# Performance work log

Measured on AMD Instinct MI355X. Metric: run time of the kernel, lower is better.

## Reference

```python
import jax, jax.numpy as jnp
import numpy as np

B, S, D, H = 4, 2048, 1024, 16
DK = D // H


def setup_inputs() -> dict:
    key = jax.random.key(0)
    ks = jax.random.split(key, 11)
    inp = {
        'query': jax.random.normal(ks[0], (B, S, D), jnp.float32),
        'key': jax.random.normal(ks[1], (B, S, D), jnp.float32),
        'value': jax.random.normal(ks[2], (B, S, D), jnp.float32),
        'mask': jnp.tril(jnp.ones((1, 1, S, S), dtype=bool)),  # causal
    }
    sc = 1.0 / np.sqrt(D)
    inp['w_q'] = jax.random.normal(ks[3], (D, D), jnp.float32) * sc
    inp['b_q'] = jnp.zeros((D,), jnp.float32)
    inp['w_k'] = jax.random.normal(ks[4], (D, D), jnp.float32) * sc
    inp['b_k'] = jnp.zeros((D,), jnp.float32)
    inp['w_v'] = jax.random.normal(ks[5], (D, D), jnp.float32) * sc
    inp['b_v'] = jnp.zeros((D,), jnp.float32)
    inp['w_o'] = jax.random.normal(ks[6], (D, D), jnp.float32) * sc
    inp['b_o'] = jnp.zeros((D,), jnp.float32)
    return inp


def _split_heads(x):
    # Faithful to source: view(B, S, d_k, H) then permute(0,3,1,2)
    b, s, _ = x.shape
    return x.reshape(b, s, DK, H).transpose(0, 3, 1, 2)  # (B, H, S, DK)


def _concat_heads(x):
    # permute(0,2,1,3) -> reshape(B, S, d_k*H)
    b, h, s, dk = x.shape
    return x.transpose(0, 2, 1, 3).reshape(b, s, dk * h)


def reference(query, key, value, mask, w_q, b_q, w_k, b_k, w_v, b_v, w_o, b_o):
    q = query @ w_q.T + b_q
    k = key @ w_k.T + b_k
    v = value @ w_v.T + b_v
    q, k, v = _split_heads(q), _split_heads(k), _split_heads(v)
    scale = 1.0 / jnp.sqrt(jnp.asarray(DK, q.dtype))
    scores = jnp.einsum('bhqd,bhkd->bhqk', q, k) * scale
    scores = jnp.where(mask, scores, -jnp.inf)
    attn = jax.nn.softmax(scores, axis=-1)  # dropout p=0 -> identity
    out = jnp.einsum('bhqk,bhkd->bhqd', attn, v)
    return _concat_heads(out) @ w_o.T + b_o
```

## Files before the change

kernel.cpp:

```cpp
#include <hip/hip_runtime.h>

#define BB 4
#define SS 2048
#define DD 1024
#define HH 16
#define DK 64
#define MM (BB * SS)

typedef __bf16 bf16x8 __attribute__((ext_vector_type(8)));
typedef float f32x4 __attribute__((ext_vector_type(4)));
typedef unsigned short us8 __attribute__((ext_vector_type(8)));
typedef unsigned short us4 __attribute__((ext_vector_type(4)));

#define MFMA_BF16(a, b, c) __builtin_amdgcn_mfma_f32_16x16x32_bf16((a), (b), (c), 0, 0, 0)

__device__ __forceinline__ unsigned short f2bf(float f) {
  return __builtin_bit_cast(unsigned short, (__bf16)f);
}

__device__ __forceinline__ bf16x8 ld_frag(const unsigned short* p) {
  return __builtin_bit_cast(bf16x8, *(const us8*)p);
}

__device__ __forceinline__ void gl_lds16(const unsigned short* g, unsigned short* l) {
  __builtin_amdgcn_global_load_lds((const __attribute__((address_space(1))) void*)g,
                                   (__attribute__((address_space(3))) void*)l, 16, 0, 0);
}

__global__ void cvt_weights(const float* __restrict__ w0, const float* __restrict__ w1,
                            const float* __restrict__ w2, const float* __restrict__ w3,
                            unsigned short* __restrict__ dst) {
  const float* src = (blockIdx.y == 0) ? w0 : (blockIdx.y == 1) ? w1 : (blockIdx.y == 2) ? w2 : w3;
  unsigned short* d = dst + (size_t)blockIdx.y * (DD * DD);
  int idx = (blockIdx.x * 256 + threadIdx.x) * 4;
  float4 v = *(const float4*)(src + idx);
  us4 o;
  o[0] = f2bf(v.x); o[1] = f2bf(v.y); o[2] = f2bf(v.z); o[3] = f2bf(v.w);
  *(us4*)(d + idx) = o;
}

__global__ void cvt_act(const float* __restrict__ xq, const float* __restrict__ xk,
                        const float* __restrict__ xv, unsigned short* __restrict__ dq,
                        unsigned short* __restrict__ dk, unsigned short* __restrict__ dv) {
  const float* src = (blockIdx.y == 0) ? xq : (blockIdx.y == 1) ? xk : xv;
  unsigned short* dst = (blockIdx.y == 0) ? dq : (blockIdx.y == 1) ? dk : dv;
  int idx = (blockIdx.x * 256 + threadIdx.x) * 8;
  float4 a = *(const float4*)(src + idx);
  float4 b = *(const float4*)(src + idx + 4);
  us8 o;
  o[0] = f2bf(a.x); o[1] = f2bf(a.y); o[2] = f2bf(a.z); o[3] = f2bf(a.w);
  o[4] = f2bf(b.x); o[5] = f2bf(b.y); o[6] = f2bf(b.z); o[7] = f2bf(b.w);
  *(us8*)(dst + idx) = o;
}

__global__ __launch_bounds__(256, 4) void qkv_gemm_bf(
    const unsigned short* __restrict__ xb, const unsigned short* __restrict__ w,
    const float* __restrict__ bias, unsigned short* __restrict__ outp, int mode) {
  const int m0 = blockIdx.x * 128;
  const int h0 = blockIdx.y * 2;

  __shared__ unsigned short smem[17408];
  unsigned short* sA = smem;
  unsigned short* sB = smem + 8192;

  const int tid = threadIdx.x;
  const int lane = tid & 63;
  const int wave = tid >> 6;
  const int wm = wave & 1, wn = wave >> 1;
  const int quad = lane >> 4, l16 = lane & 15;

  f32x4 acc[4][4];
#pragma unroll
  for (int i = 0; i < 4; i++)
#pragma unroll
    for (int j = 0; j < 4; j++) acc[i][j] = f32x4{0.f, 0.f, 0.f, 0.f};

  for (int k0 = 0; k0 < DD; k0 += 64) {
    __syncthreads();
#pragma unroll
    for (int j = 0; j < 4; j++) {
      int cid = tid + j * 256;
      int half = cid >> 9, rr = (cid & 511) >> 2, c8 = (cid & 3) << 3;
      gl_lds16(xb + (size_t)(m0 + rr) * DD + k0 + half * 32 + c8,
               sA + half * 4096 + rr * 32 + c8);
    }
#pragma unroll
    for (int j = 0; j < 4; j++) {
      int cid = tid + j * 256;
      int half = cid >> 9, rr = (cid & 511) >> 2, c8 = (cid & 3) << 3;
      int n = ((rr & 63) << 4) + h0 + (rr >> 6);
      gl_lds16(w + (size_t)n * DD + k0 + half * 32 + c8,
               sB + half * 4096 + rr * 32 + c8);
    }
    __syncthreads();

#pragma unroll
    for (int kk = 0; kk < 2; kk++) {
      bf16x8 af[4];
#pragma unroll
      for (int mi = 0; mi < 4; mi++)
        af[mi] = ld_frag(sA + kk * 4096 + (wm * 64 + mi * 16 + l16) * 32 + quad * 8);
#pragma unroll
      for (int ni = 0; ni < 4; ni++) {
        bf16x8 bfr = ld_frag(sB + kk * 4096 + (wn * 64 + ni * 16 + l16) * 32 + quad * 8);
#pragma unroll
        for (int mi = 0; mi < 4; mi++) acc[mi][ni] = MFMA_BF16(af[mi], bfr, acc[mi][ni]);
      }
    }
  }

  if (mode < 2) {
#pragma unroll
    for (int mi = 0; mi < 4; mi++) {
#pragma unroll
      for (int ni = 0; ni < 4; ni++) {
        int c = wn * 64 + ni * 16 + l16;
        int h = h0 + (c >> 6), dk = c & 63;
        float bvv = bias[(dk << 4) + h];
        int mg0 = m0 + wm * 64 + mi * 16 + quad * 4;
#pragma unroll
        for (int r = 0; r < 4; r++) {
          int mg = mg0 + r;
          int bb = mg >> 11, s = mg & 2047;
          size_t dst = ((size_t)((bb << 4) + h) * SS + s) * DK + dk;
          outp[dst] = f2bf(acc[mi][ni][r] + bvv);
        }
      }
    }
  } else {
    __syncthreads();
#pragma unroll
    for (int mi = 0; mi < 4; mi++) {
#pragma unroll
      for (int ni = 0; ni < 4; ni++) {
        int c = wn * 64 + ni * 16 + l16;
        int h = h0 + (c >> 6), dk = c & 63;
        float bvv = bias[(dk << 4) + h];
        int ml0 = wm * 64 + mi * 16 + quad * 4;
#pragma unroll
        for (int r = 0; r < 4; r++)
          smem[c * 136 + ml0 + r] = f2bf(acc[mi][ni][r] + bvv);
      }
    }
    __syncthreads();
    int bb = m0 >> 11;
    int sbase = m0 & 2047;
#pragma unroll
    for (int i = 0; i < 8; i++) {
      int idx = tid + i * 256;
      int c = idx >> 4, mc = (idx & 15) << 3;
      int h = h0 + (c >> 6), dk = c & 63;
      size_t dst = ((size_t)((bb << 4) + h) * DK + dk) * SS + sbase + mc;
      *(us8*)(outp + dst) = *(const us8*)(smem + c * 136 + mc);
    }
  }
}

__global__ __launch_bounds__(256, 2) void attn(
    const unsigned short* __restrict__ qh, const unsigned short* __restrict__ kh,
    const unsigned short* __restrict__ vt, unsigned short* __restrict__ outc) {
  const int bh = blockIdx.x;
  const int by = blockIdx.y;
  const int b = bh >> 4, h = bh & 15;
  const unsigned short* Qp = qh + (size_t)bh * SS * DK;
  const unsigned short* Kp = kh + (size_t)bh * SS * DK;
  const unsigned short* Vp = vt + (size_t)bh * DK * SS;

  __shared__ unsigned short sK[128 * 72];
  __shared__ unsigned short sV[64 * 136];

  const int tid = threadIdx.x;
  const int lane = tid & 63;
  const int wave = tid >> 6;
  const int quad = lane >> 4, l16 = lane & 15;
  const int wq0 = wave * 32;

  const float sl = 0.125f * 1.44269504088896f;

  for (int pass = 0; pass < 2; pass++) {
    const int qt = pass ? (15 - by) : by;
    const int q0 = qt * 128;

    bf16x8 aq[2][2];
#pragma unroll
    for (int mi = 0; mi < 2; mi++)
#pragma unroll
      for (int kk = 0; kk < 2; kk++)
        aq[mi][kk] = ld_frag(Qp + (size_t)(q0 + wq0 + mi * 16 + l16) * DK + kk * 32 + quad * 8);

    f32x4 o_acc[2][4];
    float mrowL[2], lrowL[2];
#pragma unroll
    for (int mi = 0; mi < 2; mi++) {
#pragma unroll
      for (int ni = 0; ni < 4; ni++) o_acc[mi][ni] = f32x4{0.f, 0.f, 0.f, 0.f};
      mrowL[mi] = -1e30f;
      lrowL[mi] = 0.f;
    }

    for (int kt = 0; kt <= qt; kt++) {
      const int k0 = kt * 128;
      const bool diag = (kt == qt);
      __syncthreads();
#pragma unroll
      for (int i = 0; i < 4; i++) {
        int idx = tid + i * 256;
        int row = idx >> 3, c8 = (idx & 7) << 3;
        *(us8*)(sK + row * 72 + c8) = *(const us8*)(Kp + (size_t)(k0 + row) * DK + c8);
      }
#pragma unroll
      for (int i = 0; i < 4; i++) {
        int idx = tid + i * 256;
        int row = idx >> 4, cc = (idx & 15) << 3;
        *(us8*)(sV + row * 136 + cc) = *(const us8*)(Vp + (size_t)row * SS + k0 + cc);
      }
      __syncthreads();

      f32x4 sc[2][8];
#pragma unroll
      for (int mi = 0; mi < 2; mi++)
#pragma unroll
        for (int kti = 0; kti < 8; kti++) sc[mi][kti] = f32x4{0.f, 0.f, 0.f, 0.f};
      __builtin_amdgcn_s_setprio(1);
#pragma unroll
      for (int kti = 0; kti < 8; kti++) {
#pragma unroll
        for (int kk = 0; kk < 2; kk++) {
          bf16x8 ak = ld_frag(sK + (kti * 16 + l16) * 72 + kk * 32 + quad * 8);
#pragma unroll
          for (int mi = 0; mi < 2; mi++) sc[mi][kti] = MFMA_BF16(ak, aq[mi][kk], sc[mi][kti]);
        }
      }
      __builtin_amdgcn_s_setprio(0);

      if (diag) {
#pragma unroll
        for (int mi = 0; mi < 2; mi++) {
          int ql = wq0 + mi * 16 + l16;
#pragma unroll
          for (int kti = 0; kti < 8; kti++)
#pragma unroll
            for (int r = 0; r < 4; r++) {
              int kl = kti * 16 + quad * 4 + r;
              float v = sc[mi][kti][r] * sl;
              sc[mi][kti][r] = (kl > ql) ? -1e30f : v;
            }
        }
      } else {
#pragma unroll
        for (int mi = 0; mi < 2; mi++)
#pragma unroll
          for (int kti = 0; kti < 8; kti++)
#pragma unroll
            for (int r = 0; r < 4; r++) sc[mi][kti][r] *= sl;
      }

      float alphaL[2];
#pragma unroll
      for (int mi = 0; mi < 2; mi++) {
        f32x4 vm = sc[mi][0];
#pragma unroll
        for (int kti = 1; kti < 8; kti++)
#pragma unroll
          for (int r = 0; r < 4; r++) vm[r] = fmaxf(vm[r], sc[mi][kti][r]);
        float mx = fmaxf(fmaxf(vm[0], vm[1]), fmaxf(vm[2], vm[3]));
        mx = fmaxf(mx, __shfl_xor(mx, 16, 64));
        mx = fmaxf(mx, __shfl_xor(mx, 32, 64));
        float mnew = fmaxf(mrowL[mi], mx);
        alphaL[mi] = exp2f(mrowL[mi] - mnew);
        mrowL[mi] = mnew;
      }

#pragma unroll
      for (int mi = 0; mi < 2; mi++) {
#pragma unroll
        for (int r = 0; r < 4; r++) {
          float a = __shfl(alphaL[mi], quad * 4 + r, 64);
#pragma unroll
          for (int ni = 0; ni < 4; ni++) o_acc[mi][ni][r] *= a;
        }
        us4 pk[8];
        f32x4 vs = f32x4{0.f, 0.f, 0.f, 0.f};
#pragma unroll
        for (int kti = 0; kti < 8; kti++) {
#pragma unroll
          for (int r = 0; r < 4; r++) {
            float p = exp2f(sc[mi][kti][r] - mrowL[mi]);
            vs[r] += p;
            pk[kti][r] = f2bf(p);
          }
        }
        float ls = (vs[0] + vs[1]) + (vs[2] + vs[3]);
        ls += __shfl_xor(ls, 16, 64);
        ls += __shfl_xor(ls, 32, 64);
        lrowL[mi] = lrowL[mi] * alphaL[mi] + ls;

        __builtin_amdgcn_s_setprio(1);
#pragma unroll
        for (int c = 0; c < 4; c++) {
          bf16x8 ap = __builtin_bit_cast(
              bf16x8, __builtin_shufflevector(pk[2 * c], pk[2 * c + 1], 0, 1, 2, 3, 4, 5, 6, 7));
#pragma unroll
          for (int ni = 0; ni < 4; ni++) {
            const unsigned short* vb = sV + (ni * 16 + l16) * 136 + c * 32 + quad * 4;
            us4 lo = *(const us4*)vb;
            us4 hi = *(const us4*)(vb + 16);
            bf16x8 bfr = __builtin_bit_cast(
                bf16x8, __builtin_shufflevector(lo, hi, 0, 1, 2, 3, 4, 5, 6, 7));
            o_acc[mi][ni] = MFMA_BF16(ap, bfr, o_acc[mi][ni]);
          }
        }
        __builtin_amdgcn_s_setprio(0);
      }
    }

#pragma unroll
    for (int mi = 0; mi < 2; mi++) {
#pragma unroll
      for (int r = 0; r < 4; r++) {
        float lr = __shfl(lrowL[mi], quad * 4 + r, 64);
        float inv = 1.0f / lr;
        int qg = q0 + wq0 + mi * 16 + quad * 4 + r;
        size_t rowbase = ((size_t)(b * SS + qg)) * DD + h * DK;
#pragma unroll
        for (int ni = 0; ni < 4; ni++) {
          int dk = ni * 16 + l16;
          outc[rowbase + dk] = f2bf(o_acc[mi][ni][r] * inv);
        }
      }
    }
    __syncthreads();
  }
}

__global__ __launch_bounds__(256, 4) void out_proj(
    const unsigned short* __restrict__ ac, const unsigned short* __restrict__ wo,
    const float* __restrict__ bias, float* __restrict__ out) {
  const int m0 = blockIdx.x * 128;
  const int n0 = blockIdx.y * 128;
  __shared__ unsigned short sA[8192];
  __shared__ unsigned short sB[8192];

  const int tid = threadIdx.x;
  const int lane = tid & 63;
  const int wave = tid >> 6;
  const int wm = wave & 1, wn = wave >> 1;
  const int quad = lane >> 4, l16 = lane & 15;

  f32x4 acc[4][4];
#pragma unroll
  for (int i = 0; i < 4; i++)
#pragma unroll
    for (int j = 0; j < 4; j++) acc[i][j] = f32x4{0.f, 0.f, 0.f, 0.f};

  for (int k0 = 0; k0 < DD; k0 += 64) {
    __syncthreads();
#pragma unroll
    for (int j = 0; j < 4; j++) {
      int cid = tid + j * 256;
      int half = cid >> 9;
      int rr = (cid & 511) >> 2;
      int c8 = (cid & 3) << 3;
      gl_lds16(ac + (size_t)(m0 + rr) * DD + k0 + half * 32 + c8,
               sA + half * 4096 + rr * 32 + c8);
    }
#pragma unroll
    for (int j = 0; j < 4; j++) {
      int cid = tid + j * 256;
      int half = cid >> 9;
      int rr = (cid & 511) >> 2;
      int c8 = (cid & 3) << 3;
      gl_lds16(wo + (size_t)(n0 + rr) * DD + k0 + half * 32 + c8,
               sB + half * 4096 + rr * 32 + c8);
    }
    __syncthreads();
#pragma unroll
    for (int kk = 0; kk < 2; kk++) {
      bf16x8 af[4];
#pragma unroll
      for (int mi = 0; mi < 4; mi++)
        af[mi] = ld_frag(sA + kk * 4096 + (wm * 64 + mi * 16 + l16) * 32 + quad * 8);
#pragma unroll
      for (int ni = 0; ni < 4; ni++) {
        bf16x8 bfr = ld_frag(sB + kk * 4096 + (wn * 64 + ni * 16 + l16) * 32 + quad * 8);
#pragma unroll
        for (int mi = 0; mi < 4; mi++) acc[mi][ni] = MFMA_BF16(af[mi], bfr, acc[mi][ni]);
      }
    }
  }

#pragma unroll
  for (int mi = 0; mi < 4; mi++) {
#pragma unroll
    for (int ni = 0; ni < 4; ni++) {
      int n = n0 + wn * 64 + ni * 16 + l16;
      float bvv = bias[n];
      int mg0 = m0 + wm * 64 + mi * 16 + quad * 4;
#pragma unroll
      for (int r = 0; r < 4; r++) out[(size_t)(mg0 + r) * DD + n] = acc[mi][ni][r] + bvv;
    }
  }
}

extern "C" void kernel_launch(void* const* d_in, const int* in_sizes, int n_in,
                              void* d_out, int out_size, void* d_ws, size_t ws_size,
                              hipStream_t stream) {
  const float* q_in = (const float*)d_in[0];
  const float* k_in = (const float*)d_in[1];
  const float* v_in = (const float*)d_in[2];
  const float* w_q = (const float*)d_in[4];
  const float* b_q = (const float*)d_in[5];
  const float* w_k = (const float*)d_in[6];
  const float* b_k = (const float*)d_in[7];
  const float* w_v = (const float*)d_in[8];
  const float* b_v = (const float*)d_in[9];
  const float* w_o = (const float*)d_in[10];
  const float* b_o = (const float*)d_in[11];
  float* out = (float*)d_out;

  unsigned short* ws = (unsigned short*)d_ws;
  unsigned short* wb = ws;
  unsigned short* qh = ws + (size_t)4 * 1024 * 1024;
  unsigned short* kh = ws + (size_t)12 * 1024 * 1024;
  unsigned short* vt = ws + (size_t)20 * 1024 * 1024;
  unsigned short* outc = ws + (size_t)28 * 1024 * 1024;
  unsigned short* xqb = kh;
  unsigned short* xkb = vt;
  unsigned short* xvb = outc;

  const size_t WSZ = (size_t)DD * DD;

  cvt_weights<<<dim3(1024, 4), 256, 0, stream>>>(w_q, w_k, w_v, w_o, wb);
  cvt_act<<<dim3(4096, 3), 256, 0, stream>>>(q_in, k_in, v_in, xqb, xkb, xvb);
  qkv_gemm_bf<<<dim3(64, 8), 256, 0, stream>>>(xqb, wb, b_q, qh, 0);
  qkv_gemm_bf<<<dim3(64, 8), 256, 0, stream>>>(xkb, wb + WSZ, b_k, kh, 1);
  qkv_gemm_bf<<<dim3(64, 8), 256, 0, stream>>>(xvb, wb + 2 * WSZ, b_v, vt, 2);
  attn<<<dim3(64, 8), 256, 0, stream>>>(qh, kh, vt, outc);
  out_proj<<<dim3(64, 8), 256, 0, stream>>>(outc, wb + 3 * WSZ, b_o, out);
}
```

Measured before the change: 362.7 us.

## Merge conversion and QKV launches, split attention tiles, add lazy softmax rescale

```diff
diff --git a/kernel.cpp b/kernel.cpp
--- a/kernel.cpp
+++ b/kernel.cpp
@@ -27,35 +27,49 @@
                                    (__attribute__((address_space(3))) void*)l, 16, 0, 0);
 }
 
-__global__ void cvt_weights(const float* __restrict__ w0, const float* __restrict__ w1,
-                            const float* __restrict__ w2, const float* __restrict__ w3,
-                            unsigned short* __restrict__ dst) {
-  const float* src = (blockIdx.y == 0) ? w0 : (blockIdx.y == 1) ? w1 : (blockIdx.y == 2) ? w2 : w3;
-  unsigned short* d = dst + (size_t)blockIdx.y * (DD * DD);
-  int idx = (blockIdx.x * 256 + threadIdx.x) * 4;
-  float4 v = *(const float4*)(src + idx);
-  us4 o;
-  o[0] = f2bf(v.x); o[1] = f2bf(v.y); o[2] = f2bf(v.z); o[3] = f2bf(v.w);
-  *(us4*)(d + idx) = o;
-}
-
-__global__ void cvt_act(const float* __restrict__ xq, const float* __restrict__ xk,
-                        const float* __restrict__ xv, unsigned short* __restrict__ dq,
-                        unsigned short* __restrict__ dk, unsigned short* __restrict__ dv) {
-  const float* src = (blockIdx.y == 0) ? xq : (blockIdx.y == 1) ? xk : xv;
-  unsigned short* dst = (blockIdx.y == 0) ? dq : (blockIdx.y == 1) ? dk : dv;
-  int idx = (blockIdx.x * 256 + threadIdx.x) * 8;
-  float4 a = *(const float4*)(src + idx);
-  float4 b = *(const float4*)(src + idx + 4);
-  us8 o;
-  o[0] = f2bf(a.x); o[1] = f2bf(a.y); o[2] = f2bf(a.z); o[3] = f2bf(a.w);
-  o[4] = f2bf(b.x); o[5] = f2bf(b.y); o[6] = f2bf(b.z); o[7] = f2bf(b.w);
-  *(us8*)(dst + idx) = o;
+__global__ void cvt_all(const float* __restrict__ w0, const float* __restrict__ w1,
+                        const float* __restrict__ w2, const float* __restrict__ w3,
+                        const float* __restrict__ xq, const float* __restrict__ xk,
+                        const float* __restrict__ xv, unsigned short* __restrict__ wb,
+                        unsigned short* __restrict__ dq, unsigned short* __restrict__ dk,
+                        unsigned short* __restrict__ dv) {
+  const int y = blockIdx.y;
+  if (y < 4) {
+    const float* src = (y == 0) ? w0 : (y == 1) ? w1 : (y == 2) ? w2 : w3;
+    unsigned short* d = wb + (size_t)y * (DD * DD);
+    int idx = (blockIdx.x * 256 + threadIdx.x) * 4;
+    float4 v = *(const float4*)(src + idx);
+    us4 o;
+    o[0] = f2bf(v.x); o[1] = f2bf(v.y); o[2] = f2bf(v.z); o[3] = f2bf(v.w);
+    *(us4*)(d + idx) = o;
+  } else {
+    const float* src = (y == 4) ? xq : (y == 5) ? xk : xv;
+    unsigned short* dst = (y == 4) ? dq : (y == 5) ? dk : dv;
+#pragma unroll
+    for (int i = 0; i < 4; i++) {
+      int idx = (((i * 1024 + blockIdx.x) * 256) + threadIdx.x) * 8;
+      float4 a = *(const float4*)(src + idx);
+      float4 b = *(const float4*)(src + idx + 4);
+      us8 o;
+      o[0] = f2bf(a.x); o[1] = f2bf(a.y); o[2] = f2bf(a.z); o[3] = f2bf(a.w);
+      o[4] = f2bf(b.x); o[5] = f2bf(b.y); o[6] = f2bf(b.z); o[7] = f2bf(b.w);
+      *(us8*)(dst + idx) = o;
+    }
+  }
 }
 
 __global__ __launch_bounds__(256, 4) void qkv_gemm_bf(
-    const unsigned short* __restrict__ xb, const unsigned short* __restrict__ w,
-    const float* __restrict__ bias, unsigned short* __restrict__ outp, int mode) {
+    const unsigned short* __restrict__ xq, const unsigned short* __restrict__ xk,
+    const unsigned short* __restrict__ xv, const unsigned short* __restrict__ wball,
+    const float* __restrict__ bq, const float* __restrict__ bk, const float* __restrict__ bv,
+    unsigned short* __restrict__ qh, unsigned short* __restrict__ kh,
+    unsigned short* __restrict__ vt) {
+  const int mode = blockIdx.z;
+  const unsigned short* xb = (mode == 0) ? xq : (mode == 1) ? xk : xv;
+  const unsigned short* w = wball + (size_t)mode * (DD * DD);
+  const float* bias = (mode == 0) ? bq : (mode == 1) ? bk : bv;
+  unsigned short* outp = (mode == 0) ? qh : (mode == 1) ? kh : vt;
+
   const int m0 = blockIdx.x * 128;
   const int h0 = blockIdx.y * 2;
 
@@ -156,11 +170,12 @@
   }
 }
 
-__global__ __launch_bounds__(256, 2) void attn(
+__global__ __launch_bounds__(256, 3) void attn(
     const unsigned short* __restrict__ qh, const unsigned short* __restrict__ kh,
     const unsigned short* __restrict__ vt, unsigned short* __restrict__ outc) {
   const int bh = blockIdx.x;
-  const int by = blockIdx.y;
+  const int qt = 15 - blockIdx.y;
+  const int q0 = qt * 128;
   const int b = bh >> 4, h = bh & 15;
   const unsigned short* Qp = qh + (size_t)bh * SS * DK;
   const unsigned short* Kp = kh + (size_t)bh * SS * DK;
@@ -177,159 +192,158 @@
 
   const float sl = 0.125f * 1.44269504088896f;
 
-  for (int pass = 0; pass < 2; pass++) {
-    const int qt = pass ? (15 - by) : by;
-    const int q0 = qt * 128;
-
-    bf16x8 aq[2][2];
+  bf16x8 aq[2][2];
+#pragma unroll
+  for (int mi = 0; mi < 2; mi++)
+#pragma unroll
+    for (int kk = 0; kk < 2; kk++)
+      aq[mi][kk] = ld_frag(Qp + (size_t)(q0 + wq0 + mi * 16 + l16) * DK + kk * 32 + quad * 8);
+
+  f32x4 o_acc[2][4];
+  float mrowL[2], lrowL[2];
+#pragma unroll
+  for (int mi = 0; mi < 2; mi++) {
+#pragma unroll
+    for (int ni = 0; ni < 4; ni++) o_acc[mi][ni] = f32x4{0.f, 0.f, 0.f, 0.f};
+    mrowL[mi] = -1e30f;
+    lrowL[mi] = 0.f;
+  }
+
+  for (int kt = 0; kt <= qt; kt++) {
+    const int k0 = kt * 128;
+    const bool diag = (kt == qt);
+    __syncthreads();
+#pragma unroll
+    for (int i = 0; i < 4; i++) {
+      int idx = tid + i * 256;
+      int row = idx >> 3, c8 = (idx & 7) << 3;
+      *(us8*)(sK + row * 72 + c8) = *(const us8*)(Kp + (size_t)(k0 + row) * DK + c8);
+    }
+#pragma unroll
+    for (int i = 0; i < 4; i++) {
+      int idx = tid + i * 256;
+      int row = idx >> 4, cc = (idx & 15) << 3;
+      *(us8*)(sV + row * 136 + cc) = *(const us8*)(Vp + (size_t)row * SS + k0 + cc);
+    }
+    __syncthreads();
+
+    f32x4 sc[2][8];
 #pragma unroll
     for (int mi = 0; mi < 2; mi++)
 #pragma unroll
-      for (int kk = 0; kk < 2; kk++)
-        aq[mi][kk] = ld_frag(Qp + (size_t)(q0 + wq0 + mi * 16 + l16) * DK + kk * 32 + quad * 8);
-
-    f32x4 o_acc[2][4];
-    float mrowL[2], lrowL[2];
+      for (int kti = 0; kti < 8; kti++) sc[mi][kti] = f32x4{0.f, 0.f, 0.f, 0.f};
+    __builtin_amdgcn_s_setprio(1);
+#pragma unroll
+    for (int kti = 0; kti < 8; kti++) {
+#pragma unroll
+      for (int kk = 0; kk < 2; kk++) {
+        bf16x8 ak = ld_frag(sK + (kti * 16 + l16) * 72 + kk * 32 + quad * 8);
+#pragma unroll
+        for (int mi = 0; mi < 2; mi++) sc[mi][kti] = MFMA_BF16(ak, aq[mi][kk], sc[mi][kti]);
+      }
+    }
+    __builtin_amdgcn_s_setprio(0);
+
+    if (diag) {
+#pragma unroll
+      for (int mi = 0; mi < 2; mi++) {
+        int ql = wq0 + mi * 16 + l16;
+#pragma unroll
+        for (int kti = 0; kti < 8; kti++)
+#pragma unroll
+          for (int r = 0; r < 4; r++) {
+            int kl = kti * 16 + quad * 4 + r;
+            if (kl > ql) sc[mi][kti][r] = -1e30f;
+          }
+      }
+    }
+
+    float alphaL[2];
+    int upd[2];
 #pragma unroll
     for (int mi = 0; mi < 2; mi++) {
-#pragma unroll
-      for (int ni = 0; ni < 4; ni++) o_acc[mi][ni] = f32x4{0.f, 0.f, 0.f, 0.f};
-      mrowL[mi] = -1e30f;
-      lrowL[mi] = 0.f;
-    }
-
-    for (int kt = 0; kt <= qt; kt++) {
-      const int k0 = kt * 128;
-      const bool diag = (kt == qt);
-      __syncthreads();
-#pragma unroll
-      for (int i = 0; i < 4; i++) {
-        int idx = tid + i * 256;
-        int row = idx >> 3, c8 = (idx & 7) << 3;
-        *(us8*)(sK + row * 72 + c8) = *(const us8*)(Kp + (size_t)(k0 + row) * DK + c8);
-      }
-#pragma unroll
-      for (int i = 0; i < 4; i++) {
-        int idx = tid + i * 256;
-        int row = idx >> 4, cc = (idx & 15) << 3;
-        *(us8*)(sV + row * 136 + cc) = *(const us8*)(Vp + (size_t)row * SS + k0 + cc);
-      }
-      __syncthreads();
-
-      f32x4 sc[2][8];
-#pragma unroll
-      for (int mi = 0; mi < 2; mi++)
-#pragma unroll
-        for (int kti = 0; kti < 8; kti++) sc[mi][kti] = f32x4{0.f, 0.f, 0.f, 0.f};
-      __builtin_amdgcn_s_setprio(1);
-#pragma unroll
-      for (int kti = 0; kti < 8; kti++) {
-#pragma unroll
-        for (int kk = 0; kk < 2; kk++) {
-          bf16x8 ak = ld_frag(sK + (kti * 16 + l16) * 72 + kk * 32 + quad * 8);
-#pragma unroll
-          for (int mi = 0; mi < 2; mi++) sc[mi][kti] = MFMA_BF16(ak, aq[mi][kk], sc[mi][kti]);
-        }
-      }
-      __builtin_amdgcn_s_setprio(0);
-
-      if (diag) {
-#pragma unroll
-        for (int mi = 0; mi < 2; mi++) {
-          int ql = wq0 + mi * 16 + l16;
-#pragma unroll
-          for (int kti = 0; kti < 8; kti++)
-#pragma unroll
-            for (int r = 0; r < 4; r++) {
-              int kl = kti * 16 + quad * 4 + r;
-              float v = sc[mi][kti][r] * sl;
-              sc[mi][kti][r] = (kl > ql) ? -1e30f : v;
-            }
-        }
-      } else {
-#pragma unroll
-        for (int mi = 0; mi < 2; mi++)
-#pragma unroll
-          for (int kti = 0; kti < 8; kti++)
-#pragma unroll
-            for (int r = 0; r < 4; r++) sc[mi][kti][r] *= sl;
-      }
-
-      float alphaL[2];
-#pragma unroll
-      for (int mi = 0; mi < 2; mi++) {
-        f32x4 vm = sc[mi][0];
-#pragma unroll
-        for (int kti = 1; kti < 8; kti++)
-#pragma unroll
-          for (int r = 0; r < 4; r++) vm[r] = fmaxf(vm[r], sc[mi][kti][r]);
-        float mx = fmaxf(fmaxf(vm[0], vm[1]), fmaxf(vm[2], vm[3]));
-        mx = fmaxf(mx, __shfl_xor(mx, 16, 64));
-        mx = fmaxf(mx, __shfl_xor(mx, 32, 64));
-        float mnew = fmaxf(mrowL[mi], mx);
+      f32x4 vm;
+#pragma unroll
+      for (int r = 0; r < 4; r++) {
+        float a0 = fmaxf(fmaxf(sc[mi][0][r], sc[mi][1][r]), sc[mi][2][r]);
+        float a1 = fmaxf(fmaxf(sc[mi][3][r], sc[mi][4][r]), sc[mi][5][r]);
+        float a2 = fmaxf(fmaxf(sc[mi][6][r], sc[mi][7][r]), a0);
+        vm[r] = fmaxf(a1, a2);
+      }
+      float mx = fmaxf(fmaxf(vm[0], vm[1]), fmaxf(vm[2], vm[3]));
+      mx = fmaxf(mx, __shfl_xor(mx, 16, 64));
+      mx = fmaxf(mx, __shfl_xor(mx, 32, 64));
+      float mxs = mx * sl;
+      upd[mi] = __any(mxs - mrowL[mi] > 8.0f);
+      if (upd[mi]) {
+        float mnew = fmaxf(mrowL[mi], mxs);
         alphaL[mi] = exp2f(mrowL[mi] - mnew);
         mrowL[mi] = mnew;
-      }
-
-#pragma unroll
-      for (int mi = 0; mi < 2; mi++) {
+      } else {
+        alphaL[mi] = 1.0f;
+      }
+    }
+
+#pragma unroll
+    for (int mi = 0; mi < 2; mi++) {
+      if (upd[mi]) {
 #pragma unroll
         for (int r = 0; r < 4; r++) {
           float a = __shfl(alphaL[mi], quad * 4 + r, 64);
 #pragma unroll
           for (int ni = 0; ni < 4; ni++) o_acc[mi][ni][r] *= a;
         }
-        us4 pk[8];
-        f32x4 vs = f32x4{0.f, 0.f, 0.f, 0.f};
-#pragma unroll
-        for (int kti = 0; kti < 8; kti++) {
-#pragma unroll
-          for (int r = 0; r < 4; r++) {
-            float p = exp2f(sc[mi][kti][r] - mrowL[mi]);
-            vs[r] += p;
-            pk[kti][r] = f2bf(p);
-          }
+      }
+      us4 pk[8];
+      f32x4 vs = f32x4{0.f, 0.f, 0.f, 0.f};
+      float mref = mrowL[mi];
+#pragma unroll
+      for (int kti = 0; kti < 8; kti++) {
+#pragma unroll
+        for (int r = 0; r < 4; r++) {
+          float p = exp2f(__builtin_fmaf(sc[mi][kti][r], sl, -mref));
+          vs[r] += p;
+          pk[kti][r] = f2bf(p);
         }
-        float ls = (vs[0] + vs[1]) + (vs[2] + vs[3]);
-        ls += __shfl_xor(ls, 16, 64);
-        ls += __shfl_xor(ls, 32, 64);
-        lrowL[mi] = lrowL[mi] * alphaL[mi] + ls;
-
-        __builtin_amdgcn_s_setprio(1);
-#pragma unroll
-        for (int c = 0; c < 4; c++) {
-          bf16x8 ap = __builtin_bit_cast(
-              bf16x8, __builtin_shufflevector(pk[2 * c], pk[2 * c + 1], 0, 1, 2, 3, 4, 5, 6, 7));
-#pragma unroll
-          for (int ni = 0; ni < 4; ni++) {
-            const unsigned short* vb = sV + (ni * 16 + l16) * 136 + c * 32 + quad * 4;
-            us4 lo = *(const us4*)vb;
-            us4 hi = *(const us4*)(vb + 16);
-            bf16x8 bfr = __builtin_bit_cast(
-                bf16x8, __builtin_shufflevector(lo, hi, 0, 1, 2, 3, 4, 5, 6, 7));
-            o_acc[mi][ni] = MFMA_BF16(ap, bfr, o_acc[mi][ni]);
-          }
+      }
+      float ls = (vs[0] + vs[1]) + (vs[2] + vs[3]);
+      ls += __shfl_xor(ls, 16, 64);
+      ls += __shfl_xor(ls, 32, 64);
+      lrowL[mi] = lrowL[mi] * alphaL[mi] + ls;
+
+      __builtin_amdgcn_s_setprio(1);
+#pragma unroll
+      for (int c = 0; c < 4; c++) {
+        bf16x8 ap = __builtin_bit_cast(
+            bf16x8, __builtin_shufflevector(pk[2 * c], pk[2 * c + 1], 0, 1, 2, 3, 4, 5, 6, 7));
+#pragma unroll
+        for (int ni = 0; ni < 4; ni++) {
+          const unsigned short* vb = sV + (ni * 16 + l16) * 136 + c * 32 + quad * 4;
+          us4 lo = *(const us4*)vb;
+          us4 hi = *(const us4*)(vb + 16);
+          bf16x8 bfr = __builtin_bit_cast(
+              bf16x8, __builtin_shufflevector(lo, hi, 0, 1, 2, 3, 4, 5, 6, 7));
+          o_acc[mi][ni] = MFMA_BF16(ap, bfr, o_acc[mi][ni]);
         }
-        __builtin_amdgcn_s_setprio(0);
-      }
-    }
-
-#pragma unroll
-    for (int mi = 0; mi < 2; mi++) {
-#pragma unroll
-      for (int r = 0; r < 4; r++) {
-        float lr = __shfl(lrowL[mi], quad * 4 + r, 64);
-        float inv = 1.0f / lr;
-        int qg = q0 + wq0 + mi * 16 + quad * 4 + r;
-        size_t rowbase = ((size_t)(b * SS + qg)) * DD + h * DK;
-#pragma unroll
-        for (int ni = 0; ni < 4; ni++) {
-          int dk = ni * 16 + l16;
-          outc[rowbase + dk] = f2bf(o_acc[mi][ni][r] * inv);
-        }
-      }
-    }
-    __syncthreads();
+      }
+      __builtin_amdgcn_s_setprio(0);
+    }
+  }
+
+#pragma unroll
+  for (int mi = 0; mi < 2; mi++) {
+#pragma unroll
+    for (int r = 0; r < 4; r++) {
+      float lr = __shfl(lrowL[mi], quad * 4 + r, 64);
+      float inv = 1.0f / lr;
+      int qg = q0 + wq0 + mi * 16 + quad * 4 + r;
+      size_t rowbase = ((size_t)(b * SS + qg)) * DD + h * DK;
+#pragma unroll
+      for (int ni = 0; ni < 4; ni++) {
+        int dk = ni * 16 + l16;
+        outc[rowbase + dk] = f2bf(o_acc[mi][ni][r] * inv);
+      }
+    }
   }
 }
 
@@ -424,17 +438,13 @@
   unsigned short* kh = ws + (size_t)12 * 1024 * 1024;
   unsigned short* vt = ws + (size_t)20 * 1024 * 1024;
   unsigned short* outc = ws + (size_t)28 * 1024 * 1024;
-  unsigned short* xqb = kh;
-  unsigned short* xkb = vt;
+  unsigned short* xqb = (unsigned short*)d_out;
+  unsigned short* xkb = (unsigned short*)d_out + (size_t)8 * 1024 * 1024;
   unsigned short* xvb = outc;
 
-  const size_t WSZ = (size_t)DD * DD;
-
-  cvt_weights<<<dim3(1024, 4), 256, 0, stream>>>(w_q, w_k, w_v, w_o, wb);
-  cvt_act<<<dim3(4096, 3), 256, 0, stream>>>(q_in, k_in, v_in, xqb, xkb, xvb);
-  qkv_gemm_bf<<<dim3(64, 8), 256, 0, stream>>>(xqb, wb, b_q, qh, 0);
-  qkv_gemm_bf<<<dim3(64, 8), 256, 0, stream>>>(xkb, wb + WSZ, b_k, kh, 1);
-  qkv_gemm_bf<<<dim3(64, 8), 256, 0, stream>>>(xvb, wb + 2 * WSZ, b_v, vt, 2);
-  attn<<<dim3(64, 8), 256, 0, stream>>>(qh, kh, vt, outc);
-  out_proj<<<dim3(64, 8), 256, 0, stream>>>(outc, wb + 3 * WSZ, b_o, out);
-}
+  cvt_all<<<dim3(1024, 7), 256, 0, stream>>>(w_q, w_k, w_v, w_o, q_in, k_in, v_in,
+                                             wb, xqb, xkb, xvb);
+  qkv_gemm_bf<<<dim3(64, 8, 3), 256, 0, stream>>>(xqb, xkb, xvb, wb, b_q, b_k, b_v, qh, kh, vt);
+  attn<<<dim3(64, 16), 256, 0, stream>>>(qh, kh, vt, outc);
+  out_proj<<<dim3(64, 8), 256, 0, stream>>>(outc, wb + 3 * (size_t)(DD * DD), b_o, out);
+}
```

Result: faster. 355.6 us (-2.0%).
